# Optimization experiments

Hardware: AMD Instinct MI355X
Metric: run time of the kernel (lower is better)

The kernel has to match this reference:

```python
import jax, jax.numpy as jnp
import numpy as np


def conv_transpose_4s2p1(x, w, b):
    # torch ConvTranspose2d(k=4, s=2, p=1). w is torch layout [Cin, Cout, 4, 4].
    # Equivalent to a regular conv with lhs_dilation=2, per-side pad k-1-p=2,
    # spatially-flipped kernel and in/out channels swapped.
    wk = jnp.flip(w, (2, 3)).transpose(1, 0, 2, 3)  # [Cout, Cin, 4, 4]
    y = jax.lax.conv_general_dilated(
        x, wk, window_strides=(1, 1), padding=((2, 2), (2, 2)),
        lhs_dilation=(2, 2), dimension_numbers=('NCHW', 'OIHW', 'NCHW'))
    return y + b[None, :, None, None]


def pac_conv_transpose_3s1p1(y, guide, w, b):
    # PacConvTranspose2d(k=3, s=1, p=1): with stride 1 this equals pacconv2d on
    # input zero-padded by k-1-p = 1, with the weight in/out-permuted and flipped
    # (pacnet native impl). Adaptive kernel: K_kk = exp(-0.5*||g_nbr - g_center||^2)
    # computed on the (zero-padded) guide at output resolution.
    B, C, H, W = y.shape
    wk = jnp.flip(w, (2, 3)).transpose(1, 0, 2, 3)  # [Cout, Cin, 3, 3]
    Co = wk.shape[0]
    gp = jnp.pad(guide, ((0, 0), (0, 0), (1, 1), (1, 1)))
    yp = jnp.pad(y, ((0, 0), (0, 0), (1, 1), (1, 1)))
    out = jnp.zeros((B, Co, H, W), y.dtype)
    for i in range(3):  # fixed 3x3 taps, not a data-dim loop
        for j in range(3):
            gn = gp[:, :, i:i + H, j:j + W]                # [B,Cg,H,W] neighbor
            d = gn - guide
            k = jnp.exp(-0.5 * jnp.sum(d * d, axis=1))      # [B,H,W] gaussian kernel
            yn = yp[:, :, i:i + H, j:j + W]                # [B,C,H,W]
            out = out + jnp.einsum('oc,bchw->bohw', wk[:, :, i, j], yn * k[:, None])
    return out + b[None, :, None, None]


def setup_inputs() -> dict:
    key = jax.random.key(0)
    k1, k2, k3, k4, k5, k6 = jax.random.split(key, 6)
    B, Cin, Cout, H, W = 4, 256, 128, 64, 64
    x = jax.random.normal(k1, (B, Cin, H, W), jnp.float32)
    # guide scaled so ||diff||^2 over 128 channels stays O(1-10) and the
    # gaussian kernel is not numerically degenerate
    guide = 0.08 * jax.random.normal(k2, (B, Cout, 2 * H, 2 * W), jnp.float32)
    w1 = jax.random.normal(k3, (Cin, Cout, 4, 4), jnp.float32) / np.sqrt(Cin * 16)
    b1 = 0.01 * jax.random.normal(k4, (Cout,), jnp.float32)
    w2 = jax.random.normal(k5, (Cout, Cout, 3, 3), jnp.float32) / np.sqrt(Cout * 9)
    b2 = 0.01 * jax.random.normal(k6, (Cout,), jnp.float32)
    return {'x': x, 'guide': guide, 'w1': w1, 'b1': b1, 'w2': w2, 'b2': b2}


def reference(x, guide, w1, b1, w2, b2):
    y = conv_transpose_4s2p1(x, w1, b1)          # [B, Cout, 2H, 2W]
    out = pac_conv_transpose_3s1p1(y, guide, w2, b2)
    return out
```

## Files before the change

### kernel.cpp

```cpp
#include <hip/hip_runtime.h>

#define B_  4
#define C1  256
#define C2  128
#define HH  64
#define WW  64
#define H2  128
#define W2  128

using short8  = __attribute__((ext_vector_type(8))) short;
using floatx4 = __attribute__((ext_vector_type(4))) float;
typedef unsigned short ushort_t;

#define W1C_OFF 0u
#define W1C_ELEMS (4 * 4 * 128 * 256)
#define W2C_OFF (W1C_ELEMS * 2u)
#define W2C_ELEMS (9 * 128 * 128)
#define KG_OFF  (W2C_OFF + W2C_ELEMS * 2u)
#define KG_ELEMS (B_ * H2 * 9 * W2)
#define XT_OFF  (KG_OFF + KG_ELEMS * 4u)
#define XT_ELEMS (B_ * HH * WW * C1)
#define Y_OFF   (XT_OFF + XT_ELEMS * 2u)
#define Y_ELEMS (B_ * H2 * W2 * C2)

static __device__ __forceinline__ ushort_t f2bf(float f) {
    union { float f; unsigned u; } v; v.f = f;
    unsigned r = v.u + 0x7FFFu + ((v.u >> 16) & 1u);
    return (ushort_t)(r >> 16);
}

__global__ void w1c_kernel(const float* __restrict__ w1, ushort_t* __restrict__ w1c) {
    int i = blockIdx.x * 256 + threadIdx.x;
    const int ci  = i & 255;
    const int co  = (i >> 8) & 127;
    const int tap = (i >> 15) & 3;
    const int cls = i >> 17;
    const int kh  = (cls >> 1) + 2 * (tap >> 1);
    const int kw  = (cls & 1) + 2 * (tap & 1);
    w1c[i] = f2bf(w1[((ci * C2 + co) * 4 + kh) * 4 + kw]);
}

__global__ void w2c_kernel(const float* __restrict__ w2, ushort_t* __restrict__ w2c) {
    int i = blockIdx.x * 256 + threadIdx.x;
    const int ci  = i & 127;
    const int o   = (i >> 7) & 127;
    const int tap = i >> 14;
    const int fi  = 2 - tap / 3;
    const int fj  = 2 - tap % 3;
    w2c[i] = f2bf(w2[((ci * C2 + o) * 3 + fi) * 3 + fj]);
}

__global__ __launch_bounds__(256) void xt_kernel(const float* __restrict__ x,
                                                 ushort_t* __restrict__ xT) {
    const int ih = blockIdx.x;
    const int b  = blockIdx.y;
    const int tid = threadIdx.x;
    __shared__ ushort_t tile[64 * 72];

    for (int chunk = 0; chunk < 4; ++chunk) {
        const int ci0 = chunk * 64;
        if (chunk) __syncthreads();
#pragma unroll
        for (int it = 0; it < 16; ++it) {
            const int cc = it * 4 + (tid >> 6);
            const int iw = tid & 63;
            const float v = x[(((size_t)b * C1 + ci0 + cc) * HH + ih) * WW + iw];
            tile[iw * 72 + cc] = f2bf(v);
        }
        __syncthreads();
#pragma unroll
        for (int it = 0; it < 2; ++it) {
            const int i  = it * 256 + tid;
            const int iw = i >> 3;
            const int t  = i & 7;
            const int4 v = *reinterpret_cast<const int4*>(&tile[iw * 72 + t * 8]);
            *reinterpret_cast<int4*>(&xT[(((size_t)(b * HH + ih) * WW) + iw) * C1 + ci0 + t * 8]) = v;
        }
    }
}

__global__ __launch_bounds__(512) void k_kernel(const float* __restrict__ guide,
                                                float* __restrict__ kg) {
    const int h = blockIdx.x;
    const int b = blockIdx.y;
    const int tid = threadIdx.x;
    const int cq  = tid >> 7;
    const int n   = tid & 127;

    float acc[9];
#pragma unroll
    for (int t = 0; t < 9; ++t) acc[t] = 0.f;

    const float* gb = guide + (size_t)b * C2 * H2 * W2;
    for (int c = cq * 32; c < cq * 32 + 32; ++c) {
        const float* grow = gb + (c * H2 + h) * W2;
        const float gc = grow[n];
#pragma unroll
        for (int di = 0; di < 3; ++di) {
            const int hh = h + di - 1;
            const bool rv = (hh >= 0) && (hh < H2);
            const float* gr = gb + (c * H2 + (rv ? hh : 0)) * W2;
#pragma unroll
            for (int dj = 0; dj < 3; ++dj) {
                const int col = n + dj - 1;
                const bool cv = rv && (col >= 0) && (col < W2);
                const float gn = cv ? gr[col] : 0.f;
                const float d = gn - gc;
                acc[di * 3 + dj] += d * d;
            }
        }
    }

    __shared__ float part[4][9][128];
#pragma unroll
    for (int t = 0; t < 9; ++t) part[cq][t][n] = acc[t];
    __syncthreads();

    for (int i = tid; i < 1152; i += 512) {
        const int t  = i >> 7;
        const int nn = i & 127;
        const float s = part[0][t][nn] + part[1][t][nn] + part[2][t][nn] + part[3][t][nn];
        kg[(size_t)(b * H2 + h) * 1152 + i] = __expf(-0.5f * s);
    }
}

__global__ __launch_bounds__(256, 2) void deconv_mfma(const ushort_t* __restrict__ xT,
                                                      const ushort_t* __restrict__ w1c,
                                                      const float* __restrict__ b1,
                                                      ushort_t* __restrict__ y) {
    const int pwc = blockIdx.x;
    const int pr  = blockIdx.y;
    const int b   = blockIdx.z;
    const int base_oh = (pr >> 1) * 4 + (pr & 1);
    const int p    = (base_oh + 1) & 1;
    const int ihA0 = (base_oh + 1 - p) >> 1;
    const int pwp  = 1 - pwc;
    const int cls  = p * 2 + pwp;

    const int tid  = threadIdx.x;
    const int lane = tid & 63;
    const int wave = tid >> 6;
    const int wm   = (wave & 1) * 64;
    const int wn   = (wave >> 1) * 64;
    const int quad = lane >> 4;
    const int l15  = lane & 15;

    __shared__ __align__(16) ushort_t lds[2 * 128 * 72];
    ushort_t* As = lds;
    ushort_t* Bs = lds + 128 * 72;

    floatx4 acc[4][4];
#pragma unroll
    for (int mi = 0; mi < 4; ++mi)
#pragma unroll
        for (int ni = 0; ni < 4; ++ni) acc[mi][ni] = (floatx4)0.f;

    for (int kc = 0; kc < 4; ++kc) {
        const int ci0 = kc * 64;
        for (int tap = 0; tap < 4; ++tap) {
            const int th = tap >> 1, tw = tap & 1;
            __syncthreads();
#pragma unroll
            for (int it = 0; it < 4; ++it) {
                const int i   = it * 256 + tid;
                const int row = i >> 3;
                const int t   = i & 7;
                const int4 v = *reinterpret_cast<const int4*>(
                    &w1c[((size_t)(cls * 4 + tap) * 128 + row) * 256 + ci0 + t * 8]);
                *reinterpret_cast<int4*>(&As[row * 72 + t * 8]) = v;
            }
#pragma unroll
            for (int it = 0; it < 4; ++it) {
                const int i   = it * 256 + tid;
                const int row = i >> 3;
                const int t   = i & 7;
                const int rh  = row >> 6;
                const int n64 = row & 63;
                const int ih  = ihA0 + rh - th;
                const int iw  = n64 + pwc - tw;
                int4 v = make_int4(0, 0, 0, 0);
                if (ih >= 0 && ih < HH && iw >= 0 && iw < WW)
                    v = *reinterpret_cast<const int4*>(
                        &xT[(((size_t)(b * HH + ih) * WW) + iw) * C1 + ci0 + t * 8]);
                *reinterpret_cast<int4*>(&Bs[row * 72 + t * 8]) = v;
            }
            __syncthreads();
#pragma unroll
            for (int k2 = 0; k2 < 2; ++k2) {
                short8 af[4], bfr[4];
#pragma unroll
                for (int mi = 0; mi < 4; ++mi)
                    af[mi] = *reinterpret_cast<const short8*>(
                        &As[(wm + mi * 16 + l15) * 72 + k2 * 32 + quad * 8]);
#pragma unroll
                for (int ni = 0; ni < 4; ++ni)
                    bfr[ni] = *reinterpret_cast<const short8*>(
                        &Bs[(wn + ni * 16 + l15) * 72 + k2 * 32 + quad * 8]);
#pragma unroll
                for (int mi = 0; mi < 4; ++mi)
#pragma unroll
                    for (int ni = 0; ni < 4; ++ni)
                        acc[mi][ni] = __builtin_amdgcn_mfma_f32_16x16x32_bf16(
                            af[mi], bfr[ni], acc[mi][ni], 0, 0, 0);
            }
        }
    }

    __syncthreads();
    ushort_t* Ot = lds;
#pragma unroll
    for (int mi = 0; mi < 4; ++mi)
#pragma unroll
        for (int ni = 0; ni < 4; ++ni) {
            const int n = wn + ni * 16 + l15;
#pragma unroll
            for (int r = 0; r < 4; ++r) {
                const int co = wm + mi * 16 + quad * 4 + r;
                Ot[n * 136 + co] = f2bf(acc[mi][ni][r] + b1[co]);
            }
        }
    __syncthreads();
#pragma unroll
    for (int it = 0; it < 8; ++it) {
        const int i   = it * 256 + tid;
        const int n   = i >> 4;
        const int t   = i & 15;
        const int rh  = n >> 6;
        const int n64 = n & 63;
        const int oh  = base_oh + 2 * rh;
        const int ow  = 2 * n64 + pwc;
        const int4 v = *reinterpret_cast<const int4*>(&Ot[n * 136 + t * 8]);
        *reinterpret_cast<int4*>(&y[(((size_t)(b * H2 + oh) * W2) + ow) * C2 + t * 8]) = v;
    }
}

__global__ __launch_bounds__(256, 2) void pac_mfma(const ushort_t* __restrict__ y,
                                                   const float* __restrict__ kg,
                                                   const ushort_t* __restrict__ w2c,
                                                   const float* __restrict__ b2,
                                                   float* __restrict__ out) {
    const int h = blockIdx.x;
    const int b = blockIdx.y;

    const int tid  = threadIdx.x;
    const int lane = tid & 63;
    const int wave = tid >> 6;
    const int wm   = (wave & 1) * 64;
    const int wn   = (wave >> 1) * 64;
    const int quad = lane >> 4;
    const int l15  = lane & 15;

    __shared__ __align__(16) ushort_t As[128 * 136];
    __shared__ __align__(16) ushort_t Ys[130 * 136];
    __shared__ float k_lds[9 * 128];

    for (int i = tid; i < 1152; i += 256)
        k_lds[i] = kg[(size_t)(b * H2 + h) * 1152 + i];

    float out_acc[4][4][4];
#pragma unroll
    for (int mi = 0; mi < 4; ++mi)
#pragma unroll
        for (int ni = 0; ni < 4; ++ni)
#pragma unroll
            for (int r = 0; r < 4; ++r) out_acc[mi][ni][r] = 0.f;

    for (int di = 0; di < 3; ++di) {
        const int hh = h + di - 1;
        if (hh < 0 || hh >= H2) continue;
        __syncthreads();
#pragma unroll
        for (int it = 0; it < 8; ++it) {
            const int i  = it * 256 + tid;
            const int r  = i >> 4;
            const int t  = i & 15;
            const int4 v = *reinterpret_cast<const int4*>(
                &y[(((size_t)(b * H2 + hh) * W2) + r) * C2 + t * 8]);
            *reinterpret_cast<int4*>(&Ys[(r + 1) * 136 + t * 8]) = v;
        }
        if (tid < 32) {
            const int ra = (tid < 16) ? 0 : 129;
            const int t  = tid & 15;
            *reinterpret_cast<int4*>(&Ys[ra * 136 + t * 8]) = make_int4(0, 0, 0, 0);
        }

        for (int dj = 0; dj < 3; ++dj) {
            const int tap = di * 3 + dj;
            __syncthreads();
#pragma unroll
            for (int it = 0; it < 8; ++it) {
                const int i   = it * 256 + tid;
                const int row = i >> 4;
                const int t   = i & 15;
                const int4 v = *reinterpret_cast<const int4*>(
                    &w2c[((size_t)tap * 128 + row) * 128 + t * 8]);
                *reinterpret_cast<int4*>(&As[row * 136 + t * 8]) = v;
            }
            __syncthreads();

            floatx4 acc[4][4];
#pragma unroll
            for (int mi = 0; mi < 4; ++mi)
#pragma unroll
                for (int ni = 0; ni < 4; ++ni) acc[mi][ni] = (floatx4)0.f;

#pragma unroll
            for (int kc = 0; kc < 4; ++kc) {
                short8 af[4], bfr[4];
#pragma unroll
                for (int mi = 0; mi < 4; ++mi)
                    af[mi] = *reinterpret_cast<const short8*>(
                        &As[(wm + mi * 16 + l15) * 136 + kc * 32 + quad * 8]);
#pragma unroll
                for (int ni = 0; ni < 4; ++ni)
                    bfr[ni] = *reinterpret_cast<const short8*>(
                        &Ys[(wn + ni * 16 + l15 + dj) * 136 + kc * 32 + quad * 8]);
#pragma unroll
                for (int mi = 0; mi < 4; ++mi)
#pragma unroll
                    for (int ni = 0; ni < 4; ++ni)
                        acc[mi][ni] = __builtin_amdgcn_mfma_f32_16x16x32_bf16(
                            af[mi], bfr[ni], acc[mi][ni], 0, 0, 0);
            }
            float kv[4];
#pragma unroll
            for (int ni = 0; ni < 4; ++ni)
                kv[ni] = k_lds[tap * 128 + wn + ni * 16 + l15];
#pragma unroll
            for (int mi = 0; mi < 4; ++mi)
#pragma unroll
                for (int ni = 0; ni < 4; ++ni)
#pragma unroll
                    for (int r = 0; r < 4; ++r)
                        out_acc[mi][ni][r] += kv[ni] * acc[mi][ni][r];
        }
    }

#pragma unroll
    for (int mi = 0; mi < 4; ++mi)
#pragma unroll
        for (int ni = 0; ni < 4; ++ni) {
            const int w = wn + ni * 16 + l15;
#pragma unroll
            for (int r = 0; r < 4; ++r) {
                const int o = wm + mi * 16 + quad * 4 + r;
                out[(((size_t)b * C2 + o) * H2 + h) * W2 + w] = out_acc[mi][ni][r] + b2[o];
            }
        }
}

extern "C" void kernel_launch(void* const* d_in, const int* in_sizes, int n_in,
                              void* d_out, int out_size, void* d_ws, size_t ws_size,
                              hipStream_t stream) {
    const float* x     = (const float*)d_in[0];
    const float* guide = (const float*)d_in[1];
    const float* w1    = (const float*)d_in[2];
    const float* b1    = (const float*)d_in[3];
    const float* w2    = (const float*)d_in[4];
    const float* b2    = (const float*)d_in[5];
    float* out = (float*)d_out;

    ushort_t* w1c = (ushort_t*)((char*)d_ws + W1C_OFF);
    ushort_t* w2c = (ushort_t*)((char*)d_ws + W2C_OFF);
    float*    kg  = (float*)((char*)d_ws + KG_OFF);
    ushort_t* xT  = (ushort_t*)((char*)d_ws + XT_OFF);
    ushort_t* y   = (ushort_t*)((char*)d_ws + Y_OFF);

    w1c_kernel<<<W1C_ELEMS / 256, 256, 0, stream>>>(w1, w1c);
    w2c_kernel<<<W2C_ELEMS / 256, 256, 0, stream>>>(w2, w2c);
    xt_kernel<<<dim3(HH, B_), 256, 0, stream>>>(x, xT);
    k_kernel<<<dim3(H2, B_), 512, 0, stream>>>(guide, kg);
    deconv_mfma<<<dim3(2, 64, B_), 256, 0, stream>>>(xT, w1c, b1, y);
    pac_mfma<<<dim3(H2, B_), 256, 0, stream>>>(y, kg, w2c, b2, out);
}
```

Measured before the change: 209.9 us.

## Reuse input halo tiles in LDS, stream weights from global, double-buffer PAC rows

In the deconv kernel, each K-chunk now loads one XOR-swizzled halo tile of input pixels into LDS and reuses it for all four taps. Weight fragments are read straight from global memory instead of being staged, which removes three of every four barrier/load phases. In the PAC kernel, y rows go into a swizzled double-buffered LDS area through async global_load_lds, so the next row prefetches while the current one computes. Weights there are also read directly from global, and the block index is swizzled for locality. The risk is more global/L2 traffic for the weight fragments in the inner MFMA loop, and LDS-occupancy changes.

```diff
diff --git a/kernel.cpp b/kernel.cpp
--- a/kernel.cpp
+++ b/kernel.cpp
@@ -11,6 +11,9 @@
 using short8  = __attribute__((ext_vector_type(8))) short;
 using floatx4 = __attribute__((ext_vector_type(4))) float;
 typedef unsigned short ushort_t;
+
+#define GLOBAL_AS __attribute__((address_space(1)))
+#define LDS_AS    __attribute__((address_space(3)))
 
 #define W1C_OFF 0u
 #define W1C_ELEMS (4 * 4 * 128 * 256)
@@ -145,9 +148,7 @@
     const int quad = lane >> 4;
     const int l15  = lane & 15;
 
-    __shared__ __align__(16) ushort_t lds[2 * 128 * 72];
-    ushort_t* As = lds;
-    ushort_t* Bs = lds + 128 * 72;
+    __shared__ __align__(16) ushort_t lds[128 * 136];
 
     floatx4 acc[4][4];
 #pragma unroll
@@ -155,47 +156,49 @@
 #pragma unroll
         for (int ni = 0; ni < 4; ++ni) acc[mi][ni] = (floatx4)0.f;
 
+    const int ihbase = ihA0 - 1;
+    const int iwbase = pwc - 1;
+
     for (int kc = 0; kc < 4; ++kc) {
-        const int ci0 = kc * 64;
-        for (int tap = 0; tap < 4; ++tap) {
-            const int th = tap >> 1, tw = tap & 1;
-            __syncthreads();
-#pragma unroll
-            for (int it = 0; it < 4; ++it) {
-                const int i   = it * 256 + tid;
-                const int row = i >> 3;
-                const int t   = i & 7;
-                const int4 v = *reinterpret_cast<const int4*>(
-                    &w1c[((size_t)(cls * 4 + tap) * 128 + row) * 256 + ci0 + t * 8]);
-                *reinterpret_cast<int4*>(&As[row * 72 + t * 8]) = v;
-            }
-#pragma unroll
-            for (int it = 0; it < 4; ++it) {
-                const int i   = it * 256 + tid;
-                const int row = i >> 3;
-                const int t   = i & 7;
-                const int rh  = row >> 6;
-                const int n64 = row & 63;
-                const int ih  = ihA0 + rh - th;
-                const int iw  = n64 + pwc - tw;
+        __syncthreads();
+#pragma unroll
+        for (int it = 0; it < 7; ++it) {
+            const int i = it * 256 + tid;
+            if (i < 1584) {
+                const int pix  = i >> 3;
+                const int c    = i & 7;
+                const int prow = pix / 66;
+                const int pcol = pix - prow * 66;
+                const int ih = ihbase + prow;
+                const int iw = iwbase + pcol;
                 int4 v = make_int4(0, 0, 0, 0);
                 if (ih >= 0 && ih < HH && iw >= 0 && iw < WW)
                     v = *reinterpret_cast<const int4*>(
-                        &xT[(((size_t)(b * HH + ih) * WW) + iw) * C1 + ci0 + t * 8]);
-                *reinterpret_cast<int4*>(&Bs[row * 72 + t * 8]) = v;
-            }
-            __syncthreads();
+                        &xT[(((size_t)(b * HH + ih) * WW) + iw) * C1 + kc * 64
+                            + ((c ^ (pcol & 7)) << 3)]);
+                *reinterpret_cast<int4*>(&lds[pix * 64 + (c << 3)]) = v;
+            }
+        }
+        __syncthreads();
+#pragma unroll
+        for (int tap = 0; tap < 4; ++tap) {
+            const int th = tap >> 1, tw = tap & 1;
 #pragma unroll
             for (int k2 = 0; k2 < 2; ++k2) {
                 short8 af[4], bfr[4];
 #pragma unroll
                 for (int mi = 0; mi < 4; ++mi)
                     af[mi] = *reinterpret_cast<const short8*>(
-                        &As[(wm + mi * 16 + l15) * 72 + k2 * 32 + quad * 8]);
-#pragma unroll
-                for (int ni = 0; ni < 4; ++ni)
+                        &w1c[((size_t)(cls * 4 + tap) * 128 + wm + mi * 16 + l15) * 256
+                             + kc * 64 + k2 * 32 + quad * 8]);
+#pragma unroll
+                for (int ni = 0; ni < 4; ++ni) {
+                    const int n   = wn + ni * 16 + l15;
+                    const int prw = (n >> 6) - th + 1;
+                    const int pcl = (n & 63) + 1 - tw;
                     bfr[ni] = *reinterpret_cast<const short8*>(
-                        &Bs[(wn + ni * 16 + l15) * 72 + k2 * 32 + quad * 8]);
+                        &lds[(prw * 66 + pcl) * 64 + (((k2 * 4 + quad) ^ (pcl & 7)) << 3)]);
+                }
 #pragma unroll
                 for (int mi = 0; mi < 4; ++mi)
 #pragma unroll
@@ -239,8 +242,10 @@
                                                    const ushort_t* __restrict__ w2c,
                                                    const float* __restrict__ b2,
                                                    float* __restrict__ out) {
-    const int h = blockIdx.x;
-    const int b = blockIdx.y;
+    const int bid = blockIdx.x;
+    const int swz = ((bid & 7) << 6) + (bid >> 3);
+    const int h = swz & 127;
+    const int b = swz >> 7;
 
     const int tid  = threadIdx.x;
     const int lane = tid & 63;
@@ -250,13 +255,34 @@
     const int quad = lane >> 4;
     const int l15  = lane & 15;
 
-    __shared__ __align__(16) ushort_t As[128 * 136];
-    __shared__ __align__(16) ushort_t Ys[130 * 136];
+    __shared__ __align__(16) ushort_t Ylds[2][130 * 128];
     __shared__ float k_lds[9 * 128];
 
+    {
+        const int zb = tid >> 7, zr = (tid >> 6) & 1, zw = tid & 63;
+        *reinterpret_cast<int*>(&Ylds[zb][(zr ? 129 : 0) * 128 + zw * 2]) = 0;
+    }
     for (int i = tid; i < 1152; i += 256)
         k_lds[i] = kg[(size_t)(b * H2 + h) * 1152 + i];
 
+    const int dlo = (h == 0) ? 1 : 0;
+    const int dhi = (h == H2 - 1) ? 1 : 2;
+
+    {
+        const ushort_t* ysrc = y + (size_t)(b * H2 + (h + dlo - 1)) * W2 * C2;
+        ushort_t* dst = &Ylds[0][128];
+#pragma unroll
+        for (int it = 0; it < 8; ++it) {
+            const int i = it * 256 + tid;
+            const int r = i >> 4;
+            const int c = i & 15;
+            const ushort_t* src = ysrc + r * C2 + ((c ^ ((r + 1) & 7)) << 3);
+            __builtin_amdgcn_global_load_lds((const GLOBAL_AS void*)src,
+                                             (LDS_AS void*)(dst + i * 8), 16, 0, 0);
+        }
+    }
+    __syncthreads();
+
     float out_acc[4][4][4];
 #pragma unroll
     for (int mi = 0; mi < 4; ++mi)
@@ -265,39 +291,25 @@
 #pragma unroll
             for (int r = 0; r < 4; ++r) out_acc[mi][ni][r] = 0.f;
 
-    for (int di = 0; di < 3; ++di) {
-        const int hh = h + di - 1;
-        if (hh < 0 || hh >= H2) continue;
-        __syncthreads();
-#pragma unroll
-        for (int it = 0; it < 8; ++it) {
-            const int i  = it * 256 + tid;
-            const int r  = i >> 4;
-            const int t  = i & 15;
-            const int4 v = *reinterpret_cast<const int4*>(
-                &y[(((size_t)(b * H2 + hh) * W2) + r) * C2 + t * 8]);
-            *reinterpret_cast<int4*>(&Ys[(r + 1) * 136 + t * 8]) = v;
-        }
-        if (tid < 32) {
-            const int ra = (tid < 16) ? 0 : 129;
-            const int t  = tid & 15;
-            *reinterpret_cast<int4*>(&Ys[ra * 136 + t * 8]) = make_int4(0, 0, 0, 0);
-        }
-
+    int cur = 0;
+    for (int di = dlo; di <= dhi; ++di) {
+        if (di < dhi) {
+            const ushort_t* ysrc = y + (size_t)(b * H2 + (h + di)) * W2 * C2;
+            ushort_t* dst = &Ylds[cur ^ 1][128];
+#pragma unroll
+            for (int it = 0; it < 8; ++it) {
+                const int i = it * 256 + tid;
+                const int r = i >> 4;
+                const int c = i & 15;
+                const ushort_t* src = ysrc + r * C2 + ((c ^ ((r + 1) & 7)) << 3);
+                __builtin_amdgcn_global_load_lds((const GLOBAL_AS void*)src,
+                                                 (LDS_AS void*)(dst + i * 8), 16, 0, 0);
+            }
+        }
+        const ushort_t* Yc = Ylds[cur];
+#pragma unroll
         for (int dj = 0; dj < 3; ++dj) {
             const int tap = di * 3 + dj;
-            __syncthreads();
-#pragma unroll
-            for (int it = 0; it < 8; ++it) {
-                const int i   = it * 256 + tid;
-                const int row = i >> 4;
-                const int t   = i & 15;
-                const int4 v = *reinterpret_cast<const int4*>(
-                    &w2c[((size_t)tap * 128 + row) * 128 + t * 8]);
-                *reinterpret_cast<int4*>(&As[row * 136 + t * 8]) = v;
-            }
-            __syncthreads();
-
             floatx4 acc[4][4];
 #pragma unroll
             for (int mi = 0; mi < 4; ++mi)
@@ -310,11 +322,14 @@
 #pragma unroll
                 for (int mi = 0; mi < 4; ++mi)
                     af[mi] = *reinterpret_cast<const short8*>(
-                        &As[(wm + mi * 16 + l15) * 136 + kc * 32 + quad * 8]);
-#pragma unroll
-                for (int ni = 0; ni < 4; ++ni)
+                        &w2c[((size_t)(tap * 128 + wm + mi * 16 + l15)) * 128
+                             + kc * 32 + quad * 8]);
+#pragma unroll
+                for (int ni = 0; ni < 4; ++ni) {
+                    const int R = wn + ni * 16 + l15 + dj;
                     bfr[ni] = *reinterpret_cast<const short8*>(
-                        &Ys[(wn + ni * 16 + l15 + dj) * 136 + kc * 32 + quad * 8]);
+                        &Yc[R * 128 + (((kc * 4 + quad) ^ (R & 7)) << 3)]);
+                }
 #pragma unroll
                 for (int mi = 0; mi < 4; ++mi)
 #pragma unroll
@@ -334,6 +349,8 @@
                     for (int r = 0; r < 4; ++r)
                         out_acc[mi][ni][r] += kv[ni] * acc[mi][ni][r];
         }
+        __syncthreads();
+        cur ^= 1;
     }
 
 #pragma unroll
@@ -371,5 +388,5 @@
     xt_kernel<<<dim3(HH, B_), 256, 0, stream>>>(x, xT);
     k_kernel<<<dim3(H2, B_), 512, 0, stream>>>(guide, kg);
     deconv_mfma<<<dim3(2, 64, B_), 256, 0, stream>>>(xT, w1c, b1, y);
-    pac_mfma<<<dim3(H2, B_), 256, 0, stream>>>(y, kg, w2c, b2, out);
-}
+    pac_mfma<<<512, 256, 0, stream>>>(y, kg, w2c, b2, out);
+}
```

After: 263.5 us. +25.6%, slower.

## Process two output rows per PAC block with swizzled LDS slabs and direct weight loads

Applied to the files above, without the earlier changes.

The PAC kernel now runs 512 threads per block and computes two output rows, staging four y rows once into XOR-swizzled LDS slabs so neighbouring rows share data. Weights are pre-swizzled in w2c and copied global-to-LDS with global_load_lds, which shares each weight tap across both rows and drops the padded stride. Boundary padding is handled by masking fragments instead of zero rows. Shared memory grows to about 160KB, which limits blocks per CU, and each tap still needs two barriers around the weight reload.

```diff
diff --git a/kernel.cpp b/kernel.cpp
--- a/kernel.cpp
+++ b/kernel.cpp
@@ -11,6 +11,9 @@
 using short8  = __attribute__((ext_vector_type(8))) short;
 using floatx4 = __attribute__((ext_vector_type(4))) float;
 typedef unsigned short ushort_t;
+
+#define GLOBAL_AS __attribute__((address_space(1)))
+#define LDS_AS    __attribute__((address_space(3)))
 
 #define W1C_OFF 0u
 #define W1C_ELEMS (4 * 4 * 128 * 256)
@@ -47,7 +50,8 @@
     const int tap = i >> 14;
     const int fi  = 2 - tap / 3;
     const int fj  = 2 - tap % 3;
-    w2c[i] = f2bf(w2[((ci * C2 + o) * 3 + fi) * 3 + fj]);
+    const int gs  = ((((ci >> 3) ^ (o & 7)) << 3) | (ci & 7));
+    w2c[tap * 16384 + o * 128 + gs] = f2bf(w2[((ci * C2 + o) * 3 + fi) * 3 + fj]);
 }
 
 __global__ __launch_bounds__(256) void xt_kernel(const float* __restrict__ x,
@@ -234,28 +238,50 @@
     }
 }
 
-__global__ __launch_bounds__(256, 2) void pac_mfma(const ushort_t* __restrict__ y,
+__global__ __launch_bounds__(512, 2) void pac_mfma(const ushort_t* __restrict__ y,
                                                    const float* __restrict__ kg,
                                                    const ushort_t* __restrict__ w2c,
                                                    const float* __restrict__ b2,
                                                    float* __restrict__ out) {
-    const int h = blockIdx.x;
-    const int b = blockIdx.y;
+    const int hblk = blockIdx.x;
+    const int b    = blockIdx.y;
+    const int h0   = hblk * 2;
 
     const int tid  = threadIdx.x;
     const int lane = tid & 63;
     const int wave = tid >> 6;
-    const int wm   = (wave & 1) * 64;
-    const int wn   = (wave >> 1) * 64;
+    const int rsub = wave >> 2;
+    const int q    = wave & 3;
+    const int wm   = (q & 1) * 64;
+    const int wn   = (q >> 1) * 64;
     const int quad = lane >> 4;
     const int l15  = lane & 15;
-
-    __shared__ __align__(16) ushort_t As[128 * 136];
-    __shared__ __align__(16) ushort_t Ys[130 * 136];
-    __shared__ float k_lds[9 * 128];
-
-    for (int i = tid; i < 1152; i += 256)
-        k_lds[i] = kg[(size_t)(b * H2 + h) * 1152 + i];
+    const int h    = h0 + rsub;
+
+    __shared__ __align__(16) ushort_t SLAB[4][128 * 128];
+    __shared__ __align__(16) ushort_t AS[128 * 128];
+
+#pragma unroll 1
+    for (int s = 0; s < 4; ++s) {
+        const int hh = h0 - 1 + s;
+        if (hh < 0 || hh >= H2) continue;
+        const ushort_t* ysrc = y + (size_t)(b * H2 + hh) * W2 * C2;
+#pragma unroll
+        for (int it = 0; it < 4; ++it) {
+            const int i = it * 512 + tid;
+            const int w = i >> 4;
+            const int c = i & 15;
+            const int4 v = *reinterpret_cast<const int4*>(&ysrc[i * 8]);
+            *reinterpret_cast<int4*>(&SLAB[s][w * 128 + ((c ^ (w & 7)) << 3)]) = v;
+        }
+    }
+#pragma unroll
+    for (int it = 0; it < 4; ++it) {
+        const int i = it * 512 + tid;
+        __builtin_amdgcn_global_load_lds((const GLOBAL_AS void*)(w2c + i * 8),
+                                         (LDS_AS void*)(&AS[i * 8]), 16, 0, 0);
+    }
+    __syncthreads();
 
     float out_acc[4][4][4];
 #pragma unroll
@@ -265,38 +291,19 @@
 #pragma unroll
             for (int r = 0; r < 4; ++r) out_acc[mi][ni][r] = 0.f;
 
+#pragma unroll 1
     for (int di = 0; di < 3; ++di) {
-        const int hh = h + di - 1;
-        if (hh < 0 || hh >= H2) continue;
-        __syncthreads();
-#pragma unroll
-        for (int it = 0; it < 8; ++it) {
-            const int i  = it * 256 + tid;
-            const int r  = i >> 4;
-            const int t  = i & 15;
-            const int4 v = *reinterpret_cast<const int4*>(
-                &y[(((size_t)(b * H2 + hh) * W2) + r) * C2 + t * 8]);
-            *reinterpret_cast<int4*>(&Ys[(r + 1) * 136 + t * 8]) = v;
-        }
-        if (tid < 32) {
-            const int ra = (tid < 16) ? 0 : 129;
-            const int t  = tid & 15;
-            *reinterpret_cast<int4*>(&Ys[ra * 136 + t * 8]) = make_int4(0, 0, 0, 0);
-        }
-
+        const int hh  = h + di - 1;
+        const bool hok = (hh >= 0) && (hh < H2);
+        const ushort_t* SB = &SLAB[rsub + di][0];
+#pragma unroll 1
         for (int dj = 0; dj < 3; ++dj) {
             const int tap = di * 3 + dj;
-            __syncthreads();
-#pragma unroll
-            for (int it = 0; it < 8; ++it) {
-                const int i   = it * 256 + tid;
-                const int row = i >> 4;
-                const int t   = i & 15;
-                const int4 v = *reinterpret_cast<const int4*>(
-                    &w2c[((size_t)tap * 128 + row) * 128 + t * 8]);
-                *reinterpret_cast<int4*>(&As[row * 136 + t * 8]) = v;
-            }
-            __syncthreads();
+
+            float kv[4];
+#pragma unroll
+            for (int ni = 0; ni < 4; ++ni)
+                kv[ni] = kg[(size_t)(b * H2 + h) * 1152 + tap * 128 + wn + ni * 16 + l15];
 
             floatx4 acc[4][4];
 #pragma unroll
@@ -308,13 +315,20 @@
             for (int kc = 0; kc < 4; ++kc) {
                 short8 af[4], bfr[4];
 #pragma unroll
-                for (int mi = 0; mi < 4; ++mi)
+                for (int mi = 0; mi < 4; ++mi) {
+                    const int row = wm + mi * 16 + l15;
                     af[mi] = *reinterpret_cast<const short8*>(
-                        &As[(wm + mi * 16 + l15) * 136 + kc * 32 + quad * 8]);
-#pragma unroll
-                for (int ni = 0; ni < 4; ++ni)
-                    bfr[ni] = *reinterpret_cast<const short8*>(
-                        &Ys[(wn + ni * 16 + l15 + dj) * 136 + kc * 32 + quad * 8]);
+                        &AS[row * 128 + (((kc * 4 + quad) ^ (row & 7)) << 3)]);
+                }
+#pragma unroll
+                for (int ni = 0; ni < 4; ++ni) {
+                    const int col  = wn + ni * 16 + l15 + dj - 1;
+                    const int colc = col & 127;
+                    const short8 t = *reinterpret_cast<const short8*>(
+                        &SB[colc * 128 + (((kc * 4 + quad) ^ (colc & 7)) << 3)]);
+                    const bool ok = hok && (col >= 0) && (col < W2);
+                    bfr[ni] = ok ? t : (short8)0;
+                }
 #pragma unroll
                 for (int mi = 0; mi < 4; ++mi)
 #pragma unroll
@@ -322,10 +336,6 @@
                         acc[mi][ni] = __builtin_amdgcn_mfma_f32_16x16x32_bf16(
                             af[mi], bfr[ni], acc[mi][ni], 0, 0, 0);
             }
-            float kv[4];
-#pragma unroll
-            for (int ni = 0; ni < 4; ++ni)
-                kv[ni] = k_lds[tap * 128 + wn + ni * 16 + l15];
 #pragma unroll
             for (int mi = 0; mi < 4; ++mi)
 #pragma unroll
@@ -333,6 +343,18 @@
 #pragma unroll
                     for (int r = 0; r < 4; ++r)
                         out_acc[mi][ni][r] += kv[ni] * acc[mi][ni][r];
+
+            if (tap < 8) {
+                __syncthreads();
+                const ushort_t* wsrc = w2c + (size_t)(tap + 1) * 16384;
+#pragma unroll
+                for (int it = 0; it < 4; ++it) {
+                    const int i = it * 512 + tid;
+                    __builtin_amdgcn_global_load_lds((const GLOBAL_AS void*)(wsrc + i * 8),
+                                                     (LDS_AS void*)(&AS[i * 8]), 16, 0, 0);
+                }
+                __syncthreads();
+            }
         }
     }
 
@@ -371,5 +393,5 @@
     xt_kernel<<<dim3(HH, B_), 256, 0, stream>>>(x, xT);
     k_kernel<<<dim3(H2, B_), 512, 0, stream>>>(guide, kg);
     deconv_mfma<<<dim3(2, 64, B_), 256, 0, stream>>>(xT, w1c, b1, y);
-    pac_mfma<<<dim3(H2, B_), 256, 0, stream>>>(y, kg, w2c, b2, out);
-}
+    pac_mfma<<<dim3(64, B_), 512, 0, stream>>>(y, kg, w2c, b2, out);
+}
```

Measured after the change: 199.8 us. 4.8% less time.
